# Kernel optimization log

Hardware: AMD Instinct MI355X
Metric: run time of the kernel (lower is better)

The kernel has to match this reference:

```python
import jax, jax.numpy as jnp
import numpy as np

N_NODES = 50000
N_EDGES = 800000
NUM_IN, NUM_HID, NUM_OUT = 512, 256, 64
EPS = 1e-12


def agnn_conv(x, src, dst, beta, num_nodes):
    # PyG AGNNConv: score(j->i) = beta * cos(x_i, x_j); softmax over incoming
    # edges of each target node i; out_i = sum_j alpha_ij * x_j.
    norm = jnp.maximum(jnp.linalg.norm(x, axis=1, keepdims=True), EPS)
    xn = x / norm                                      # [N, H]
    scores = beta * jnp.sum(xn[dst] * xn[src], axis=1)  # [E]
    m = jax.ops.segment_max(scores, dst, num_segments=num_nodes)
    e = jnp.exp(scores - m[dst])
    s = jax.ops.segment_sum(e, dst, num_segments=num_nodes)
    alpha = e / s[dst]                                  # [E]
    return jax.ops.segment_sum(alpha[:, None] * x[src], dst, num_segments=num_nodes)


def setup_inputs() -> dict:
    key = jax.random.key(0)
    ks = jax.random.split(key, 7)
    x = jax.random.normal(ks[0], (N_NODES, NUM_IN), dtype=jnp.float32)
    edge_index = jax.random.randint(ks[1], (2, N_EDGES), 0, N_NODES, dtype=jnp.int64)
    w1 = jax.random.normal(ks[2], (NUM_HID, NUM_IN), dtype=jnp.float32) / np.sqrt(NUM_IN)
    b1 = jnp.zeros((NUM_HID,), dtype=jnp.float32)
    beta2 = jnp.ones((1,), dtype=jnp.float32)
    w2 = jax.random.normal(ks[3], (NUM_OUT, NUM_HID), dtype=jnp.float32) / np.sqrt(NUM_HID)
    b2 = jnp.zeros((NUM_OUT,), dtype=jnp.float32)
    return {"x": x, "edge_index": edge_index, "w1": w1, "b1": b1,
            "beta2": beta2, "w2": w2, "b2": b2}


def reference(x, edge_index, w1, b1, beta2, w2, b2):
    n = x.shape[0]
    # add self-loops (PyG AGNNConv default add_self_loops=True)
    loops = jnp.arange(n, dtype=edge_index.dtype)
    src = jnp.concatenate([edge_index[0], loops])
    dst = jnp.concatenate([edge_index[1], loops])

    h = jax.nn.relu(x @ w1.T + b1)                       # [N, H] (eval: dropout = id)
    h = agnn_conv(h, src, dst, jnp.float32(1.0), n)      # prop1, fixed beta=1
    z1 = h
    h = agnn_conv(h, src, dst, beta2[0], n)              # prop2, learnable beta
    z2 = h
    logits = h @ w2.T + b2                               # [N, C]
    return (z1, z2, jax.nn.log_softmax(logits, axis=1))
```

## Files before the change

### kernel.cpp

```cpp
#include <hip/hip_runtime.h>

#define N_NODES 50000
#define N_EDGES 800000
#define ETOT (N_EDGES + N_NODES)
#define DIN 512
#define HID 256
#define NOUT 64
#define SCAN_CHUNK 2048

typedef __attribute__((ext_vector_type(8))) short short8;
typedef __attribute__((ext_vector_type(4))) float f32x4;
typedef __attribute__((ext_vector_type(2))) float f32x2;
typedef __attribute__((ext_vector_type(4))) unsigned short us4;

#define FMA2(a, b, c) __builtin_elementwise_fma((a), (b), (c))

__device__ __forceinline__ unsigned short f2bf(float f) {
  union { float f; unsigned u; } x; x.f = f;
  unsigned r = x.u + 0x7fff + ((x.u >> 16) & 1);
  return (unsigned short)(r >> 16);
}
__device__ __forceinline__ float bf2f(unsigned short b) {
  return __uint_as_float(((unsigned)b) << 16);
}
__device__ __forceinline__ f32x2 bfpair(unsigned u) {
  f32x2 r;
  r.x = __uint_as_float(u << 16);
  r.y = __uint_as_float(u & 0xffff0000u);
  return r;
}

#define AS1(p) ((const __attribute__((address_space(1))) unsigned int*)(p))
#define AS3(p) ((__attribute__((address_space(3))) unsigned int*)(p))

__device__ __forceinline__ int edge_at(const void* ei, long long idx, int is32) {
  if (is32) return ((const int*)ei)[idx];
  return (int)((const long long*)ei)[idx];
}

__global__ void initK(const void* ei, int* cursor, int* flag) {
  int i = blockIdx.x * blockDim.x + threadIdx.x;
  if (i < N_NODES) cursor[i] = 1;
  if (blockIdx.x == 0 && threadIdx.x < 64) {
    int lane = threadIdx.x;
    bool bad = false;
#pragma unroll
    for (int j = 0; j < 32; ++j) {
      long long v = ((const long long*)ei)[lane * 32 + j];
      bad |= (v < 0 || v >= N_NODES);
    }
    bool anybad = __any(bad);
    if (lane == 0) *flag = anybad ? 1 : 0;
  }
}

__global__ void histK(const void* ei, const int* flag, int* cursor) {
  int e = blockIdx.x * blockDim.x + threadIdx.x;
  if (e >= N_EDGES) return;
  int f = *flag;
  int d = edge_at(ei, (long long)N_EDGES + e, f);
  atomicAdd(&cursor[d], 1);
}

__global__ void scan1K(const int* counts, int* excl, int* bsums) {
  __shared__ int sdata[256];
  int base = blockIdx.x * SCAN_CHUNK;
  int t = threadIdx.x;
  int local[8];
  int sum = 0;
#pragma unroll
  for (int j = 0; j < 8; ++j) {
    int idx = base + t * 8 + j;
    int v = (idx < N_NODES) ? counts[idx] : 0;
    local[j] = sum;
    sum += v;
  }
  sdata[t] = sum;
  __syncthreads();
  for (int off = 1; off < 256; off <<= 1) {
    int v = (t >= off) ? sdata[t - off] : 0;
    __syncthreads();
    sdata[t] += v;
    __syncthreads();
  }
  int texcl = (t == 0) ? 0 : sdata[t - 1];
#pragma unroll
  for (int j = 0; j < 8; ++j) {
    int idx = base + t * 8 + j;
    if (idx < N_NODES) excl[idx] = texcl + local[j];
  }
  if (t == 255) bsums[blockIdx.x] = sdata[255];
}

__global__ void scan2K(int* bsums, int nb) {
  if (threadIdx.x == 0 && blockIdx.x == 0) {
    int run = 0;
    for (int i = 0; i < nb; ++i) { int v = bsums[i]; bsums[i] = run; run += v; }
  }
}

__global__ void scan3K(int* row_ptr, const int* bsums, int* cursor) {
  int i = blockIdx.x * blockDim.x + threadIdx.x;
  if (i < N_NODES) {
    int v = row_ptr[i] + bsums[i >> 11];
    row_ptr[i] = v;
    cursor[i] = v;
    if (i == 0) row_ptr[N_NODES] = ETOT;
  }
}

__global__ void scatterK(const void* ei, const int* flag, int* cursor, int* col) {
  int e = blockIdx.x * blockDim.x + threadIdx.x;
  if (e < N_EDGES) {
    int f = *flag;
    int s = edge_at(ei, e, f);
    int d = edge_at(ei, (long long)N_EDGES + e, f);
    int pos = atomicAdd(&cursor[d], 1);
    col[pos] = s;
  } else if (e < N_EDGES + N_NODES) {
    int i = e - N_EDGES;
    int pos = atomicAdd(&cursor[i], 1);
    col[pos] = i;
  }
}

__global__ __launch_bounds__(256) void cvtK(const float* __restrict__ x,
                                            const float* __restrict__ w1,
                                            unsigned short* __restrict__ xb,
                                            unsigned short* __restrict__ wb) {
  const long long NX = (long long)N_NODES * DIN / 8;
  const long long NW = (long long)HID * DIN / 8;
  long long stride = (long long)gridDim.x * blockDim.x;
  for (long long c = (long long)blockIdx.x * blockDim.x + threadIdx.x;
       c < NX + NW; c += stride) {
    const float* src;
    unsigned short* dst;
    if (c < NX) { src = x + c * 8; dst = xb + c * 8; }
    else { src = w1 + (c - NX) * 8; dst = wb + (c - NX) * 8; }
    float4 v0 = ((const float4*)src)[0];
    float4 v1 = ((const float4*)src)[1];
    short8 s;
    s[0] = f2bf(v0.x); s[1] = f2bf(v0.y); s[2] = f2bf(v0.z); s[3] = f2bf(v0.w);
    s[4] = f2bf(v1.x); s[5] = f2bf(v1.y); s[6] = f2bf(v1.z); s[7] = f2bf(v1.w);
    *(short8*)dst = s;
  }
}

__global__ __launch_bounds__(256) void gemm1MF(const unsigned short* __restrict__ Ab,
                                               const unsigned short* __restrict__ Bb,
                                               const float* __restrict__ bias,
                                               unsigned short* __restrict__ C) {
  __shared__ short As[128 * 64];
  __shared__ short Bs[128 * 64];
  int t = threadIdx.x;
  int wv = t >> 6, ln = t & 63;
  int wr = wv >> 1, wc = wv & 1;
  int row0 = blockIdx.x * 128;
  int col0 = blockIdx.y * 128;

  int lr = ln >> 3, lc = ln & 7;
  int scol = ((lc ^ lr) << 3);

  int ar0 = row0 + lr;
  const unsigned short* bbase = &Bb[(long long)(col0 + lr) * DIN + scol];

  f32x4 acc[4][4];
#pragma unroll
  for (int mi = 0; mi < 4; ++mi)
#pragma unroll
    for (int ni = 0; ni < 4; ++ni) acc[mi][ni] = (f32x4){0.f, 0.f, 0.f, 0.f};

  int g = ln >> 4;
  int fr = ln & 15;

  for (int k0 = 0; k0 < DIN; k0 += 64) {
#pragma unroll
    for (int it = 0; it < 4; ++it) {
      int chunk = it * 4 + wv;
      int ar = ar0 + chunk * 8;
      if (ar >= N_NODES) ar = N_NODES - 1;
      const unsigned short* asrc = &Ab[(long long)ar * DIN + k0 + scol];
      __builtin_amdgcn_global_load_lds(AS1(asrc), AS3(&As[chunk * 512]), 16, 0, 0);
      const unsigned short* bsrc = bbase + k0 + (long long)chunk * 8 * DIN;
      __builtin_amdgcn_global_load_lds(AS1(bsrc), AS3(&Bs[chunk * 512]), 16, 0, 0);
    }
    __syncthreads();

#pragma unroll
    for (int kk = 0; kk < 2; ++kk) {
      short8 af[4], bfr[4];
#pragma unroll
      for (int mi = 0; mi < 4; ++mi) {
        int r = wr * 64 + mi * 16 + fr;
        int slot = (kk * 4 + g) ^ (r & 7);
        af[mi] = *(const short8*)&As[r * 64 + slot * 8];
      }
#pragma unroll
      for (int ni = 0; ni < 4; ++ni) {
        int c = wc * 64 + ni * 16 + fr;
        int slot = (kk * 4 + g) ^ (c & 7);
        bfr[ni] = *(const short8*)&Bs[c * 64 + slot * 8];
      }
#pragma unroll
      for (int mi = 0; mi < 4; ++mi)
#pragma unroll
        for (int ni = 0; ni < 4; ++ni)
          acc[mi][ni] = __builtin_amdgcn_mfma_f32_16x16x32_bf16(af[mi], bfr[ni], acc[mi][ni], 0, 0, 0);
    }
    __syncthreads();
  }

  int fq = ln >> 4;
#pragma unroll
  for (int ni = 0; ni < 4; ++ni) {
    int colv = col0 + wc * 64 + ni * 16 + fr;
    float bv = bias[colv];
#pragma unroll
    for (int mi = 0; mi < 4; ++mi) {
#pragma unroll
      for (int j = 0; j < 4; ++j) {
        int row = row0 + wr * 64 + mi * 16 + fq * 4 + j;
        if (row < N_NODES)
          C[(long long)row * HID + colv] = f2bf(fmaxf(acc[mi][ni][j] + bv, 0.f));
      }
    }
  }
}

__global__ __launch_bounds__(256) void normBF(const unsigned short* __restrict__ hb,
                                              float* __restrict__ invn) {
  int w = (blockIdx.x * 256 + threadIdx.x) >> 6;
  int lane = threadIdx.x & 63;
  if (w >= N_NODES) return;
  us4 v = *(const us4*)&hb[(long long)w * HID + lane * 4];
  float x = bf2f(v.x), y = bf2f(v.y), z = bf2f(v.z), ww = bf2f(v.w);
  float s = x * x + y * y + z * z + ww * ww;
#pragma unroll
  for (int off = 32; off >= 1; off >>= 1) s += __shfl_xor(s, off);
  if (lane == 0) invn[w] = 1.0f / fmaxf(sqrtf(s), 1e-12f);
}

__global__ __launch_bounds__(256) void convK(const unsigned short* __restrict__ hb,
                                             const float* __restrict__ invn,
                                             const int* __restrict__ row_ptr,
                                             const int* __restrict__ col,
                                             const float* __restrict__ beta_ptr,
                                             float* __restrict__ hout,
                                             unsigned short* __restrict__ hout_bf) {
  int w = (blockIdx.x * 256 + threadIdx.x) >> 6;
  int lane = threadIdx.x & 63;
  if (w >= N_NODES) return;
  int g = lane >> 4;
  int sub = lane & 15;
  float beta = beta_ptr ? beta_ptr[0] : 1.0f;
  float babs = fabsf(beta);

  const char* hbase = (const char*)hb;
  unsigned ioff = (unsigned)w * (unsigned)(HID * 2) + (unsigned)sub * 32u;
  uint4 ia = *(const uint4*)(hbase + ioff);
  uint4 ib = *(const uint4*)(hbase + ioff + 16);
  float scale_i = invn[w] * beta;
  f32x2 hi[8];
  hi[0] = bfpair(ia.x) * scale_i; hi[1] = bfpair(ia.y) * scale_i;
  hi[2] = bfpair(ia.z) * scale_i; hi[3] = bfpair(ia.w) * scale_i;
  hi[4] = bfpair(ib.x) * scale_i; hi[5] = bfpair(ib.y) * scale_i;
  hi[6] = bfpair(ib.z) * scale_i; hi[7] = bfpair(ib.w) * scale_i;

  int e0 = row_ptr[w], e1 = row_ptr[w + 1];
  int nit = (e1 - e0 + 3) >> 2;

  int ee0 = e0 + g;
  int s = col[ee0 < e1 ? ee0 : (e1 - 1)];
  float is = invn[s];
  unsigned off = (unsigned)s * (unsigned)(HID * 2) + (unsigned)sub * 32u;
  uint4 ja = *(const uint4*)(hbase + off);
  uint4 jb = *(const uint4*)(hbase + off + 16);

  float Z = 0.f;
  f32x2 acc[8];
#pragma unroll
  for (int q = 0; q < 8; ++q) acc[q] = (f32x2){0.f, 0.f};

  for (int it = 0; it < nit; ++it) {
    bool valid = (e0 + it * 4 + g) < e1;
    int sn = s; float isn = is; uint4 jan = ja, jbn = jb;
    if (it + 1 < nit) {
      int een = e0 + (it + 1) * 4 + g;
      sn = col[een < e1 ? een : (e1 - 1)];
      isn = invn[sn];
      unsigned offn = (unsigned)sn * (unsigned)(HID * 2) + (unsigned)sub * 32u;
      jan = *(const uint4*)(hbase + offn);
      jbn = *(const uint4*)(hbase + offn + 16);
    }
    f32x2 hj[8];
    hj[0] = bfpair(ja.x); hj[1] = bfpair(ja.y);
    hj[2] = bfpair(ja.z); hj[3] = bfpair(ja.w);
    hj[4] = bfpair(jb.x); hj[5] = bfpair(jb.y);
    hj[6] = bfpair(jb.z); hj[7] = bfpair(jb.w);
    f32x2 d2 = (f32x2){0.f, 0.f};
#pragma unroll
    for (int q = 0; q < 8; ++q) d2 = FMA2(hi[q], hj[q], d2);
    float p = d2.x + d2.y;
    p += __shfl_xor(p, 1);
    p += __shfl_xor(p, 2);
    p += __shfl_xor(p, 4);
    p += __shfl_xor(p, 8);
    float sc = p * is;
    float wt = valid ? __expf(sc - babs) : 0.f;
    Z += wt;
    f32x2 w2 = (f32x2){wt, wt};
#pragma unroll
    for (int q = 0; q < 8; ++q) acc[q] = FMA2(w2, hj[q], acc[q]);
    s = sn; is = isn; ja = jan; jb = jbn;
  }

#pragma unroll
  for (int q = 0; q < 8; ++q) {
    acc[q].x += __shfl_xor(acc[q].x, 16);
    acc[q].x += __shfl_xor(acc[q].x, 32);
    acc[q].y += __shfl_xor(acc[q].y, 16);
    acc[q].y += __shfl_xor(acc[q].y, 32);
  }
  Z += __shfl_xor(Z, 16);
  Z += __shfl_xor(Z, 32);
  float r = 1.0f / Z;

  if (g == 0) {
    float* po = &hout[(long long)w * HID + sub * 16];
#pragma unroll
    for (int q4 = 0; q4 < 4; ++q4) {
      float4 o;
      o.x = acc[q4 * 2 + 0].x * r;
      o.y = acc[q4 * 2 + 0].y * r;
      o.z = acc[q4 * 2 + 1].x * r;
      o.w = acc[q4 * 2 + 1].y * r;
      *(float4*)&po[q4 * 4] = o;
    }
  } else if (g == 1 && hout_bf) {
    unsigned short* pb = &hout_bf[(long long)w * HID + sub * 16];
#pragma unroll
    for (int q4 = 0; q4 < 4; ++q4) {
      us4 ob;
      ob.x = f2bf(acc[q4 * 2 + 0].x * r);
      ob.y = f2bf(acc[q4 * 2 + 0].y * r);
      ob.z = f2bf(acc[q4 * 2 + 1].x * r);
      ob.w = f2bf(acc[q4 * 2 + 1].y * r);
      *(us4*)&pb[q4 * 4] = ob;
    }
  }
}

__global__ __launch_bounds__(256) void headK2(const float* __restrict__ Z,
                                              const float* __restrict__ W,
                                              const float* __restrict__ bias,
                                              float* __restrict__ out) {
  __shared__ float smem[2 * 32 * 68];
  float* As = smem;
  float* Bs = smem + 32 * 68;
  int t = threadIdx.x;
  int tx = t & 15, ty = t >> 4;
  int row0 = blockIdx.x * 64;
  float acc[4][4] = {};
  int lr = t >> 3;
  int lc4 = t & 7;

  for (int k0 = 0; k0 < HID; k0 += 32) {
#pragma unroll
    for (int rr = 0; rr < 64; rr += 32) {
      int gr = row0 + lr + rr;
      float4 va = (gr < N_NODES)
                      ? *(const float4*)&Z[(long long)gr * HID + k0 + lc4 * 4]
                      : make_float4(0.f, 0.f, 0.f, 0.f);
      As[(lc4 * 4 + 0) * 68 + lr + rr] = va.x;
      As[(lc4 * 4 + 1) * 68 + lr + rr] = va.y;
      As[(lc4 * 4 + 2) * 68 + lr + rr] = va.z;
      As[(lc4 * 4 + 3) * 68 + lr + rr] = va.w;
      int gc = lr + rr;
      float4 vb = *(const float4*)&W[(long long)gc * HID + k0 + lc4 * 4];
      Bs[(lc4 * 4 + 0) * 68 + lr + rr] = vb.x;
      Bs[(lc4 * 4 + 1) * 68 + lr + rr] = vb.y;
      Bs[(lc4 * 4 + 2) * 68 + lr + rr] = vb.z;
      Bs[(lc4 * 4 + 3) * 68 + lr + rr] = vb.w;
    }
    __syncthreads();
#pragma unroll
    for (int kk = 0; kk < 32; ++kk) {
      float4 a4 = *(const float4*)&As[kk * 68 + ty * 4];
      float4 b4 = *(const float4*)&Bs[kk * 68 + tx * 4];
      acc[0][0] += a4.x * b4.x; acc[0][1] += a4.x * b4.y; acc[0][2] += a4.x * b4.z; acc[0][3] += a4.x * b4.w;
      acc[1][0] += a4.y * b4.x; acc[1][1] += a4.y * b4.y; acc[1][2] += a4.y * b4.z; acc[1][3] += a4.y * b4.w;
      acc[2][0] += a4.z * b4.x; acc[2][1] += a4.z * b4.y; acc[2][2] += a4.z * b4.z; acc[2][3] += a4.z * b4.w;
      acc[3][0] += a4.w * b4.x; acc[3][1] += a4.w * b4.y; acc[3][2] += a4.w * b4.z; acc[3][3] += a4.w * b4.w;
    }
    __syncthreads();
  }

  float* ls = smem;
  float4 bv = *(const float4*)&bias[tx * 4];
#pragma unroll
  for (int r = 0; r < 4; ++r) {
    int lrow = ty * 4 + r;
    ls[lrow * 65 + tx * 4 + 0] = acc[r][0] + bv.x;
    ls[lrow * 65 + tx * 4 + 1] = acc[r][1] + bv.y;
    ls[lrow * 65 + tx * 4 + 2] = acc[r][2] + bv.z;
    ls[lrow * 65 + tx * 4 + 3] = acc[r][3] + bv.w;
  }
  __syncthreads();

  int wid = t >> 6, lane = t & 63;
#pragma unroll
  for (int rr2 = wid; rr2 < 64; rr2 += 4) {
    int node = row0 + rr2;
    if (node < N_NODES) {
      float v = ls[rr2 * 65 + lane];
      float mx = v;
#pragma unroll
      for (int off = 32; off >= 1; off >>= 1) mx = fmaxf(mx, __shfl_xor(mx, off));
      float ex = __expf(v - mx);
      float se = ex;
#pragma unroll
      for (int off = 32; off >= 1; off >>= 1) se += __shfl_xor(se, off);
      out[(long long)node * NOUT + lane] = v - mx - __logf(se);
    }
  }
}

extern "C" void kernel_launch(void* const* d_in, const int* in_sizes, int n_in,
                              void* d_out, int out_size, void* d_ws, size_t ws_size,
                              hipStream_t stream) {
  (void)in_sizes; (void)n_in; (void)out_size; (void)ws_size;
  const float* x = (const float*)d_in[0];
  const void* ei = d_in[1];
  const float* w1 = (const float*)d_in[2];
  const float* b1 = (const float*)d_in[3];
  const float* beta2 = (const float*)d_in[4];
  const float* w2 = (const float*)d_in[5];
  const float* b2 = (const float*)d_in[6];

  float* z1 = (float*)d_out;
  float* z2 = z1 + (size_t)N_NODES * HID;
  float* lsm = z2 + (size_t)N_NODES * HID;

  unsigned short* h_bf = (unsigned short*)d_ws;
  unsigned short* z1_bf = h_bf + (size_t)N_NODES * HID;
  float* invn = (float*)(z1_bf + (size_t)N_NODES * HID);
  int* row_ptr = (int*)(invn + N_NODES);
  int* cursor = row_ptr + N_NODES + 1;
  int* colv = cursor + N_NODES;
  int* bsums = colv + ETOT;
  int* flag = bsums + 64;
  unsigned short* wb = (unsigned short*)(flag + 4);

  unsigned short* xb = (unsigned short*)z2;

  int nScan = (N_NODES + SCAN_CHUNK - 1) / SCAN_CHUNK;

  cvtK<<<2048, 256, 0, stream>>>(x, w1, xb, wb);
  initK<<<(N_NODES + 255) / 256, 256, 0, stream>>>(ei, cursor, flag);

  dim3 gg((N_NODES + 127) / 128, HID / 128);
  gemm1MF<<<gg, 256, 0, stream>>>(xb, wb, b1, h_bf);

  histK<<<(N_EDGES + 255) / 256, 256, 0, stream>>>(ei, flag, cursor);
  scan1K<<<nScan, 256, 0, stream>>>(cursor, row_ptr, bsums);
  scan2K<<<1, 64, 0, stream>>>(bsums, nScan);
  scan3K<<<(N_NODES + 255) / 256, 256, 0, stream>>>(row_ptr, bsums, cursor);
  scatterK<<<(N_EDGES + N_NODES + 255) / 256, 256, 0, stream>>>(ei, flag, cursor, colv);

  normBF<<<(N_NODES + 3) / 4, 256, 0, stream>>>(h_bf, invn);
  convK<<<(N_NODES + 3) / 4, 256, 0, stream>>>(h_bf, invn, row_ptr, colv, nullptr, z1, z1_bf);
  normBF<<<(N_NODES + 3) / 4, 256, 0, stream>>>(z1_bf, invn);
  convK<<<(N_NODES + 3) / 4, 256, 0, stream>>>(z1_bf, invn, row_ptr, colv, beta2, z2, nullptr);

  headK2<<<(N_NODES + 63) / 64, 256, 0, stream>>>(z2, w2, b2, lsm);
}
```

Baseline: 369.5 us.

## Fuse second-layer norm into first conv and prefetch column indices two ahead

The first convK now computes the inverse L2 norm of its bf16-rounded output and writes it to a new buffer, so the separate normBF launch before the second conv is removed along with its re-read of z1_bf. The gather loop also loads the column index two iterations ahead, so the dependent col->row load chain is pipelined deeper, and it drops the conditional around the next-row prefetch. The cost is extra shuffles and conversions per node in the first conv, plus a few more live registers from the deeper prefetch.

```diff
diff --git a/kernel.cpp b/kernel.cpp
--- a/kernel.cpp
+++ b/kernel.cpp
@@ -246,7 +246,8 @@
                                              const int* __restrict__ col,
                                              const float* __restrict__ beta_ptr,
                                              float* __restrict__ hout,
-                                             unsigned short* __restrict__ hout_bf) {
+                                             unsigned short* __restrict__ hout_bf,
+                                             float* __restrict__ invn_out) {
   int w = (blockIdx.x * 256 + threadIdx.x) >> 6;
   int lane = threadIdx.x & 63;
   if (w >= N_NODES) return;
@@ -268,13 +269,16 @@
 
   int e0 = row_ptr[w], e1 = row_ptr[w + 1];
   int nit = (e1 - e0 + 3) >> 2;
+  int elast = e1 - 1;
 
   int ee0 = e0 + g;
-  int s = col[ee0 < e1 ? ee0 : (e1 - 1)];
-  float is = invn[s];
-  unsigned off = (unsigned)s * (unsigned)(HID * 2) + (unsigned)sub * 32u;
-  uint4 ja = *(const uint4*)(hbase + off);
-  uint4 jb = *(const uint4*)(hbase + off + 16);
+  int c0 = col[ee0 < e1 ? ee0 : elast];
+  int ee1 = e0 + 4 + g;
+  int c1 = col[ee1 < e1 ? ee1 : elast];
+  float is = invn[c0];
+  unsigned off0 = (unsigned)c0 * (unsigned)(HID * 2) + (unsigned)sub * 32u;
+  uint4 ja = *(const uint4*)(hbase + off0);
+  uint4 jb = *(const uint4*)(hbase + off0 + 16);
 
   float Z = 0.f;
   f32x2 acc[8];
@@ -283,15 +287,12 @@
 
   for (int it = 0; it < nit; ++it) {
     bool valid = (e0 + it * 4 + g) < e1;
-    int sn = s; float isn = is; uint4 jan = ja, jbn = jb;
-    if (it + 1 < nit) {
-      int een = e0 + (it + 1) * 4 + g;
-      sn = col[een < e1 ? een : (e1 - 1)];
-      isn = invn[sn];
-      unsigned offn = (unsigned)sn * (unsigned)(HID * 2) + (unsigned)sub * 32u;
-      jan = *(const uint4*)(hbase + offn);
-      jbn = *(const uint4*)(hbase + offn + 16);
-    }
+    int ee2 = e0 + (it + 2) * 4 + g;
+    int c2 = col[ee2 < e1 ? ee2 : elast];
+    float isn = invn[c1];
+    unsigned offn = (unsigned)c1 * (unsigned)(HID * 2) + (unsigned)sub * 32u;
+    uint4 jan = *(const uint4*)(hbase + offn);
+    uint4 jbn = *(const uint4*)(hbase + offn + 16);
     f32x2 hj[8];
     hj[0] = bfpair(ja.x); hj[1] = bfpair(ja.y);
     hj[2] = bfpair(ja.z); hj[3] = bfpair(ja.w);
@@ -311,7 +312,7 @@
     f32x2 w2 = (f32x2){wt, wt};
 #pragma unroll
     for (int q = 0; q < 8; ++q) acc[q] = FMA2(w2, hj[q], acc[q]);
-    s = sn; is = isn; ja = jan; jb = jbn;
+    c1 = c2; is = isn; ja = jan; jb = jbn;
   }
 
 #pragma unroll
@@ -347,6 +348,22 @@
       ob.w = f2bf(acc[q4 * 2 + 1].y * r);
       *(us4*)&pb[q4 * 4] = ob;
     }
+  }
+
+  if (invn_out) {
+    float ss = 0.f;
+#pragma unroll
+    for (int q = 0; q < 8; ++q) {
+      float vx = bf2f(f2bf(acc[q].x * r));
+      float vy = bf2f(f2bf(acc[q].y * r));
+      ss = fmaf(vx, vx, ss);
+      ss = fmaf(vy, vy, ss);
+    }
+    ss += __shfl_xor(ss, 1);
+    ss += __shfl_xor(ss, 2);
+    ss += __shfl_xor(ss, 4);
+    ss += __shfl_xor(ss, 8);
+    if (lane == 0) invn_out[w] = 1.0f / fmaxf(sqrtf(ss), 1e-12f);
   }
 }
 
@@ -450,6 +467,7 @@
   int* bsums = colv + ETOT;
   int* flag = bsums + 64;
   unsigned short* wb = (unsigned short*)(flag + 4);
+  float* invn2 = (float*)(wb + (size_t)HID * DIN);
 
   unsigned short* xb = (unsigned short*)z2;
 
@@ -468,9 +486,8 @@
   scatterK<<<(N_EDGES + N_NODES + 255) / 256, 256, 0, stream>>>(ei, flag, cursor, colv);
 
   normBF<<<(N_NODES + 3) / 4, 256, 0, stream>>>(h_bf, invn);
-  convK<<<(N_NODES + 3) / 4, 256, 0, stream>>>(h_bf, invn, row_ptr, colv, nullptr, z1, z1_bf);
-  normBF<<<(N_NODES + 3) / 4, 256, 0, stream>>>(z1_bf, invn);
-  convK<<<(N_NODES + 3) / 4, 256, 0, stream>>>(z1_bf, invn, row_ptr, colv, beta2, z2, nullptr);
+  convK<<<(N_NODES + 3) / 4, 256, 0, stream>>>(h_bf, invn, row_ptr, colv, nullptr, z1, z1_bf, invn2);
+  convK<<<(N_NODES + 3) / 4, 256, 0, stream>>>(z1_bf, invn2, row_ptr, colv, beta2, z2, nullptr, nullptr);
 
   headK2<<<(N_NODES + 63) / 64, 256, 0, stream>>>(z2, w2, b2, lsm);
 }
```

Result: faster. 359.1 us (-2.8%).
